# Performance work log

Measured on AMD Instinct MI355X. Metric: run time of the kernel, lower is better.

Reference implementation:

```python
import jax, jax.numpy as jnp
import numpy as np

EPS = 1e-6  # torch F.normalize eps


def setup_inputs() -> dict:
    key = jax.random.key(0)
    ks = jax.random.split(key, 9)
    B, C, H, W = 2, 256, 64, 64
    nH, dk, dv = 4, 64, 64
    s = 0.05  # weight scale for numerical stability
    return {
        "x": jax.random.normal(ks[0], (B, C, H, W), jnp.float32),
        "Wq": jax.random.normal(ks[1], (nH, dk, C), jnp.float32) * s,
        "bq": jax.random.normal(ks[2], (nH, dk), jnp.float32) * s,
        "Wk": jax.random.normal(ks[3], (nH, dk, C), jnp.float32) * s,
        "bk": jax.random.normal(ks[4], (nH, dk), jnp.float32) * s,
        "Wv": jax.random.normal(ks[5], (nH, dv, C), jnp.float32) * s,
        "bv": jax.random.normal(ks[6], (nH, dv), jnp.float32) * s,
        "Wm": jax.random.normal(ks[7], (C, nH * dv), jnp.float32) * s,
        "bm": jax.random.normal(ks[8], (C,), jnp.float32) * s,
    }


def _l2norm(t):
    # torch F.normalize along channel dim (axis=2 here: [B,H,dk,L])
    n = jnp.sqrt(jnp.sum(t * t, axis=2, keepdims=True))
    return t / jnp.maximum(n, EPS)


def reference(x, Wq, bq, Wk, bk, Wv, bv, Wm, bm):
    B, C, H, W = x.shape
    nH = Wq.shape[0]
    L = H * W
    xf = x.reshape(B, C, L)  # 1x1 conv == channel matmul on flattened spatial
    # per-head projections: [B, nH, d, L]
    Q = jnp.einsum('bcl,hdc->bhdl', xf, Wq) + bq[None, :, :, None]
    K = jnp.einsum('bcl,hdc->bhdl', xf, Wk) + bk[None, :, :, None]
    V = jnp.einsum('bcl,hvc->bhvl', xf, Wv) + bv[None, :, :, None]
    Q = _l2norm(Q)
    K = _l2norm(K)
    # cosine-similarity scores A[b,h,i,j] = sum_d Q[b,h,d,i] K[b,h,d,j]
    A = jnp.einsum('bhdi,bhdj->bhij', Q, K)
    A = jax.nn.softmax(A, axis=-1)
    # R[b,h,v,i] = sum_j A[b,h,i,j] V[b,h,v,j]
    R = jnp.einsum('bhij,bhvj->bhvi', A, V)
    # concat heads along channels -> [B, nH*dv, L]
    Rc = R.reshape(B, nH * V.shape[2], L)
    out = jnp.einsum('bcl,oc->bol', Rc, Wm) + bm[None, :, None]
    out = out.reshape(B, C, H, W) + x  # residual
    return out
```

## Files before the change

kernel.cpp:

```cpp
#include <hip/hip_runtime.h>
#include <hip/hip_bf16.h>
#include <cstdint>
#include <cstddef>

typedef __bf16 bf16;
typedef bf16 bf16x8 __attribute__((ext_vector_type(8)));
typedef bf16 bf16x4 __attribute__((ext_vector_type(4)));
typedef bf16 bf16x2 __attribute__((ext_vector_type(2)));
typedef float f32x4 __attribute__((ext_vector_type(4)));
typedef float f32x16 __attribute__((ext_vector_type(16)));

#define MFMA16(A, B, Cc) __builtin_amdgcn_mfma_f32_16x16x32_bf16((A), (B), (Cc), 0, 0, 0)
#define MFMA32(A, B, Cc) __builtin_amdgcn_mfma_f32_32x32x16_bf16((A), (B), (Cc), 0, 0, 0)
#define GLD16(g, l)                                                          \
  __builtin_amdgcn_global_load_lds(                                          \
      (const __attribute__((address_space(1))) void*)(g),                    \
      (__attribute__((address_space(3))) void*)(l), 16, 0, 0)

static constexpr int L   = 4096;
static constexpr int CH  = 256;
static constexpr int NH  = 4;

static constexpr size_t OFF_WALL = 0;
static constexpr size_t OFF_WMB  = 393216;
static constexpr size_t OFF_BALL = 524288;
static constexpr size_t OFF_XT   = 528384;
static constexpr size_t OFF_QT   = 4722688;
static constexpr size_t OFF_KT   = 8916992;
static constexpr size_t OFF_VD   = 13111296;
static constexpr size_t OFF_RP1  = 17305600;
static constexpr size_t OFF_RP2  = 21499904;
static constexpr size_t OFF_RP3  = 25694208;
static constexpr size_t OFF_DP4  = 29888512;
static constexpr size_t OFF_DP2  = 21499904;
static constexpr size_t NEED4    = 30412800;

__global__ __launch_bounds__(256) void k_prep(
    const float* __restrict__ Wq, const float* __restrict__ Wk,
    const float* __restrict__ Wv, const float* __restrict__ bq,
    const float* __restrict__ bk, const float* __restrict__ bv,
    const float* __restrict__ Wm, const float* __restrict__ x,
    bf16* __restrict__ Wall, float* __restrict__ ball,
    bf16* __restrict__ Wmb, bf16* __restrict__ xT) {
  __shared__ float t[32][33];
  const int bid = blockIdx.x;
  const int tid = threadIdx.x;
  if (bid < 1027) {
    int id = bid * 256 + tid;
    if (id < 65536)        Wall[id] = (bf16)Wq[id];
    else if (id < 131072)  Wall[id] = (bf16)Wk[id - 65536];
    else if (id < 196608)  Wall[id] = (bf16)Wv[id - 131072];
    else if (id < 262144)  Wmb[id - 196608] = (bf16)Wm[id - 196608];
    else if (id < 262912) {
      int k = id - 262144;
      ball[k] = (k < 256) ? bq[k] : (k < 512) ? bk[k - 256] : bv[k - 512];
    }
  } else {
    const int id = bid - 1027;
    const int b = id >> 10;
    const int c0 = ((id >> 7) & 7) * 32;
    const int l0 = (id & 127) * 32;
    const int tx = tid & 31, ty = tid >> 5;
    #pragma unroll
    for (int i = 0; i < 4; ++i) {
      int c = c0 + ty + 8 * i;
      t[ty + 8 * i][tx] = x[((size_t)b * CH + c) * L + l0 + tx];
    }
    __syncthreads();
    #pragma unroll
    for (int i = 0; i < 4; ++i) {
      int l = l0 + ty + 8 * i;
      xT[((size_t)b * L + l) * CH + c0 + tx] = (bf16)t[tx][ty + 8 * i];
    }
  }
}

__global__ __launch_bounds__(256) void k_proj(
    const bf16* __restrict__ Wall, const float* __restrict__ ball,
    const bf16* __restrict__ xT, bf16* __restrict__ Qt,
    bf16* __restrict__ Kt, bf16* __restrict__ Vd) {
  const int b = blockIdx.z, strip = blockIdx.y, lt = blockIdx.x;
  const int w = threadIdx.x >> 6;
  const int lane = threadIdx.x & 63;
  const int lo = lane & 15, g = lane >> 4;
  const int l0 = lt * 256 + w * 64;

  const bf16* wbase = Wall + (size_t)strip * 64 * CH;
  const bf16* xbase = xT + (size_t)b * L * CH;

  f32x4 acc[4][4];
  #pragma unroll
  for (int m = 0; m < 4; ++m)
    #pragma unroll
    for (int n = 0; n < 4; ++n) acc[m][n] = (f32x4){0.f, 0.f, 0.f, 0.f};

  #pragma unroll
  for (int kc = 0; kc < 8; ++kc) {
    bf16x8 aw[4], bx[4];
    #pragma unroll
    for (int m = 0; m < 4; ++m)
      aw[m] = *(const bf16x8*)(wbase + (size_t)(16 * m + lo) * CH + kc * 32 + g * 8);
    #pragma unroll
    for (int n = 0; n < 4; ++n)
      bx[n] = *(const bf16x8*)(xbase + (size_t)(l0 + 16 * n + lo) * CH + kc * 32 + g * 8);
    #pragma unroll
    for (int m = 0; m < 4; ++m)
      #pragma unroll
      for (int n = 0; n < 4; ++n) acc[m][n] = MFMA16(aw[m], bx[n], acc[m][n]);
  }

  #pragma unroll
  for (int m = 0; m < 4; ++m)
    #pragma unroll
    for (int r = 0; r < 4; ++r) {
      float bias = ball[strip * 64 + 16 * m + 4 * g + r];
      #pragma unroll
      for (int n = 0; n < 4; ++n) acc[m][n][r] += bias;
    }

  if (strip < 8) {
    #pragma unroll
    for (int n = 0; n < 4; ++n) {
      float ss = 0.f;
      #pragma unroll
      for (int m = 0; m < 4; ++m)
        #pragma unroll
        for (int r = 0; r < 4; ++r) ss += acc[m][n][r] * acc[m][n][r];
      ss += __shfl_xor(ss, 16);
      ss += __shfl_xor(ss, 32);
      float sc = 1.f / fmaxf(sqrtf(ss), 1e-6f);
      #pragma unroll
      for (int m = 0; m < 4; ++m)
        #pragma unroll
        for (int r = 0; r < 4; ++r) acc[m][n][r] *= sc;
    }
    bf16* dst = (strip < 4) ? Qt : Kt;
    const int h = strip & 3;
    #pragma unroll
    for (int n = 0; n < 4; ++n) {
      const int l = l0 + 16 * n + lo;
      #pragma unroll
      for (int m = 0; m < 4; ++m) {
        size_t base = ((size_t)(b * NH + h) * L + l) * 64 + 16 * m + 4 * g;
        bf16x2 v01, v23;
        v01[0] = (bf16)acc[m][n][0]; v01[1] = (bf16)acc[m][n][1];
        v23[0] = (bf16)acc[m][n][2]; v23[1] = (bf16)acc[m][n][3];
        *(bf16x2*)(dst + base)     = v01;
        *(bf16x2*)(dst + base + 2) = v23;
      }
    }
  } else {
    const int h = strip - 8;
    const int lop = (lo & 3) | ((lo & 4) << 1) | ((lo & 8) >> 1);
    #pragma unroll
    for (int m = 0; m < 4; ++m)
      #pragma unroll
      for (int r = 0; r < 4; ++r) {
        const int d = 16 * m + 4 * g + r;
        #pragma unroll
        for (int n = 0; n < 4; ++n) {
          const int l = l0 + 16 * n + lop;
          Vd[((size_t)(b * NH + h) * 64 + d) * L + l] = (bf16)acc[m][n][r];
        }
      }
  }
}


#define STAGE(bb, j0)                                                          \
  {                                                                            \
    const char* gk0 = kbase + (size_t)((j0) + sr) * 128 + scS;                 \
    const char* gk1 = kbase + (size_t)((j0) + 32 + sr) * 128 + scS;            \
    const char* gv0 = vbase + (size_t)sr * 8192 + (size_t)(j0) * 2 + scS;      \
    const char* gv1 = vbase + (size_t)(32 + sr) * 8192 + (size_t)(j0) * 2 + scS; \
    GLD16(gk0, kbuf[bb] + tid * 16);                                           \
    GLD16(gk1, kbuf[bb] + 4096 + tid * 16);                                    \
    GLD16(gv0, vbuf[bb] + tid * 16);                                           \
    GLD16(gv1, vbuf[bb] + 4096 + tid * 16);                                    \
  }

#define COMPUTE(bb)                                                            \
  {                                                                            \
    const char* kb = kbuf[bb];                                                 \
    const char* vb = vbuf[bb];                                                 \
    _Pragma("unroll") for (int jb = 0; jb < 2; ++jb) {                         \
      bf16x8 kf[4], vf[2][2];                                                  \
      _Pragma("unroll") for (int f = 0; f < 4; ++f)                            \
        kf[f] = *(const bf16x8*)(kb + (32 * jb + ln) * 128 +                   \
                                 ((32 * f + 16 * hi) ^ sw));                   \
      _Pragma("unroll") for (int dvb = 0; dvb < 2; ++dvb)                      \
        _Pragma("unroll") for (int c = 0; c < 2; ++c)                          \
          vf[dvb][c] = *(const bf16x8*)(vb + (32 * dvb + ln) * 128 +           \
                                        ((64 * jb + 32 * c + 16 * hi) ^ sw));  \
      _Pragma("unroll") for (int qb = 0; qb < 2; ++qb) {                       \
        f32x16 z;                                                              \
        _Pragma("unroll") for (int r = 0; r < 16; ++r) z[r] = 0.f;             \
        _Pragma("unroll") for (int f = 0; f < 4; ++f)                          \
          z = MFMA32(kf[f], qf[qb][f], z);                                     \
        float p[16];                                                           \
        _Pragma("unroll") for (int r = 0; r < 16; ++r) p[r] = __expf(z[r]);    \
        float t0 = (p[0] + p[1]) + (p[2] + p[3]);                              \
        float t1 = (p[4] + p[5]) + (p[6] + p[7]);                              \
        float t2 = (p[8] + p[9]) + (p[10] + p[11]);                            \
        float t3 = (p[12] + p[13]) + (p[14] + p[15]);                          \
        den[qb] += (t0 + t1) + (t2 + t3);                                      \
        bf16x8 pf0, pf1;                                                       \
        _Pragma("unroll") for (int e = 0; e < 8; ++e) {                        \
          pf0[e] = (bf16)p[e];                                                 \
          pf1[e] = (bf16)p[8 + e];                                             \
        }                                                                      \
        _Pragma("unroll") for (int dvb = 0; dvb < 2; ++dvb) {                  \
          racc[qb][dvb] = MFMA32(pf0, vf[dvb][0], racc[qb][dvb]);              \
          racc[qb][dvb] = MFMA32(pf1, vf[dvb][1], racc[qb][dvb]);              \
        }                                                                      \
      }                                                                        \
    }                                                                          \
  }

template <int JS>
__global__ __launch_bounds__(256, 2) void k_attn(
    const bf16* __restrict__ Qt, const bf16* __restrict__ Kt,
    const bf16* __restrict__ Vd, bf16* __restrict__ R0,
    bf16* __restrict__ R1, bf16* __restrict__ R2, bf16* __restrict__ R3,
    float* __restrict__ D0, float* __restrict__ D1,
    float* __restrict__ D2, float* __restrict__ D3) {
  const int id = blockIdx.x;
  const int bh = id & 7;
  const int qt = (id >> 3) & 15;
  const int js = id >> 7;
  const int tid = threadIdx.x;
  const int w = tid >> 6;
  const int lane = tid & 63;
  const int ln = lane & 31, hi = lane >> 5;
  const int sw = (ln & 7) << 4;
  const int i0 = qt * 256 + w * 64;

  __shared__ __align__(16) char kbuf[2][8192];
  __shared__ __align__(16) char vbuf[2][8192];

  const char* kbase = (const char*)(Kt + (size_t)bh * L * 64);
  const char* vbase = (const char*)(Vd + (size_t)bh * 64 * L);

  const int sr = tid >> 3;
  const int sc = (tid & 7) * 16;
  const int scS = sc ^ ((sr & 7) << 4);

  const bf16* qbp = Qt + ((size_t)bh * L + i0) * 64;
  bf16x8 qf[2][4];
  #pragma unroll
  for (int qb = 0; qb < 2; ++qb)
    #pragma unroll
    for (int f = 0; f < 4; ++f)
      qf[qb][f] = *(const bf16x8*)(qbp + (size_t)(32 * qb + ln) * 64 + 16 * f + 8 * hi);

  f32x16 racc[2][2];
  #pragma unroll
  for (int qb = 0; qb < 2; ++qb)
    #pragma unroll
    for (int dvb = 0; dvb < 2; ++dvb)
      #pragma unroll
      for (int r = 0; r < 16; ++r) racc[qb][dvb][r] = 0.f;
  float den[2] = {0.f, 0.f};

  const int jbeg = js * (L / JS);
  const int nt = (L / JS) / 64;

  STAGE(0, jbeg)
  __syncthreads();
  for (int it = 0; it < nt; ++it) {
    const int bb = it & 1;
    if (it + 1 < nt) STAGE(bb ^ 1, jbeg + (it + 1) * 64)
    COMPUTE(bb)
    __syncthreads();
  }

  #pragma unroll
  for (int qb = 0; qb < 2; ++qb) den[qb] += __shfl_xor(den[qb], 32);

  bf16* rp = (js == 0) ? R0 : (js == 1) ? R1 : (js == 2) ? R2 : R3;
  float* dp = (js == 0) ? D0 : (js == 1) ? D1 : (js == 2) ? D2 : D3;

  if (hi == 0) {
    #pragma unroll
    for (int qb = 0; qb < 2; ++qb)
      dp[(size_t)bh * L + i0 + 32 * qb + ln] = den[qb];
  }
  #pragma unroll
  for (int qb = 0; qb < 2; ++qb)
    #pragma unroll
    for (int dvb = 0; dvb < 2; ++dvb)
      #pragma unroll
      for (int r = 0; r < 16; ++r) {
        const int q = 32 * qb + (r & 3) + 8 * (r >> 2) + 4 * hi;
        rp[((size_t)bh * L + i0 + q) * 64 + 32 * dvb + ln] = (bf16)racc[qb][dvb][r];
      }
}

template <int JS>
__global__ __launch_bounds__(256) void k_out(
    const bf16* __restrict__ Wmb, const bf16* __restrict__ R0,
    const bf16* __restrict__ R1, const bf16* __restrict__ R2,
    const bf16* __restrict__ R3, const float* __restrict__ D0,
    const float* __restrict__ D1, const float* __restrict__ D2,
    const float* __restrict__ D3, const float* __restrict__ x,
    const float* __restrict__ bm, float* __restrict__ out) {
  const int b = blockIdx.y, lt = blockIdx.x;
  const int w = threadIdx.x >> 6;
  const int lane = threadIdx.x & 63;
  const int lo = lane & 15, g = lane >> 4;
  const int o0 = w * 64, l0 = lt * 32;

  float invd[2][4];
  #pragma unroll
  for (int n = 0; n < 2; ++n) {
    const int l = l0 + 16 * n + lo;
    #pragma unroll
    for (int h = 0; h < 4; ++h) {
      const size_t di = (size_t)(b * NH + h) * L + l;
      float dd = D0[di] + D1[di];
      if (JS == 4) dd += D2[di] + D3[di];
      invd[n][h] = 1.0f / dd;
    }
  }

  f32x4 acc[4][2];
  #pragma unroll
  for (int m = 0; m < 4; ++m)
    #pragma unroll
    for (int n = 0; n < 2; ++n) acc[m][n] = (f32x4){0.f, 0.f, 0.f, 0.f};

  #pragma unroll
  for (int kc = 0; kc < 8; ++kc) {
    bf16x8 aw[4], bx[2];
    #pragma unroll
    for (int m = 0; m < 4; ++m)
      aw[m] = *(const bf16x8*)(Wmb + (size_t)(o0 + 16 * m + lo) * CH + kc * 32 + g * 8);
    const int h = kc >> 1;
    #pragma unroll
    for (int n = 0; n < 2; ++n) {
      const size_t base = ((size_t)(b * NH + h) * L + (l0 + 16 * n + lo)) * 64 +
                          (kc & 1) * 32 + 8 * g;
      bf16x8 r0 = *(const bf16x8*)(R0 + base);
      bf16x8 r1 = *(const bf16x8*)(R1 + base);
      const float iv = invd[n][h];
      if (JS == 4) {
        bf16x8 r2 = *(const bf16x8*)(R2 + base);
        bf16x8 r3 = *(const bf16x8*)(R3 + base);
        #pragma unroll
        for (int e = 0; e < 8; ++e) {
          float s = ((float)r0[e] + (float)r1[e]) + ((float)r2[e] + (float)r3[e]);
          bx[n][e] = (bf16)(s * iv);
        }
      } else {
        #pragma unroll
        for (int e = 0; e < 8; ++e)
          bx[n][e] = (bf16)(((float)r0[e] + (float)r1[e]) * iv);
      }
    }
    #pragma unroll
    for (int m = 0; m < 4; ++m)
      #pragma unroll
      for (int n = 0; n < 2; ++n) acc[m][n] = MFMA16(aw[m], bx[n], acc[m][n]);
  }

  #pragma unroll
  for (int m = 0; m < 4; ++m)
    #pragma unroll
    for (int r = 0; r < 4; ++r) {
      const int o = o0 + 16 * m + 4 * g + r;
      const float bias = bm[o];
      #pragma unroll
      for (int n = 0; n < 2; ++n) {
        const int l = l0 + 16 * n + lo;
        size_t idx = ((size_t)b * CH + o) * (size_t)L + l;
        out[idx] = acc[m][n][r] + bias + x[idx];
      }
    }
}

extern "C" void kernel_launch(void* const* d_in, const int* in_sizes, int n_in,
                              void* d_out, int out_size, void* d_ws, size_t ws_size,
                              hipStream_t stream) {
  const float* x  = (const float*)d_in[0];
  const float* Wq = (const float*)d_in[1];
  const float* bq = (const float*)d_in[2];
  const float* Wk = (const float*)d_in[3];
  const float* bk = (const float*)d_in[4];
  const float* Wv = (const float*)d_in[5];
  const float* bv = (const float*)d_in[6];
  const float* Wm = (const float*)d_in[7];
  const float* bm = (const float*)d_in[8];
  float* out = (float*)d_out;

  char* ws = (char*)d_ws;
  bf16*  Wall = (bf16*)(ws + OFF_WALL);
  bf16*  Wmb  = (bf16*)(ws + OFF_WMB);
  float* ball = (float*)(ws + OFF_BALL);
  bf16*  xT   = (bf16*)(ws + OFF_XT);
  bf16*  Qt   = (bf16*)(ws + OFF_QT);
  bf16*  Kt   = (bf16*)(ws + OFF_KT);
  bf16*  Vd   = (bf16*)(ws + OFF_VD);

  bf16* Rp0 = (bf16*)(ws + OFF_XT);
  bf16* Rp1 = (bf16*)(ws + OFF_RP1);

  k_prep<<<3075, 256, 0, stream>>>(Wq, Wk, Wv, bq, bk, bv, Wm, x, Wall, ball, Wmb, xT);
  k_proj<<<dim3(16, 12, 2), 256, 0, stream>>>(Wall, ball, xT, Qt, Kt, Vd);

  if (ws_size >= NEED4) {
    bf16*  Rp2 = (bf16*)(ws + OFF_RP2);
    bf16*  Rp3 = (bf16*)(ws + OFF_RP3);
    float* Dp  = (float*)(ws + OFF_DP4);
    float* D0 = Dp, *D1 = Dp + 32768, *D2 = Dp + 65536, *D3 = Dp + 98304;
    k_attn<4><<<512, 256, 0, stream>>>(Qt, Kt, Vd, Rp0, Rp1, Rp2, Rp3, D0, D1, D2, D3);
    k_out<4><<<dim3(128, 2), 256, 0, stream>>>(Wmb, Rp0, Rp1, Rp2, Rp3, D0, D1, D2, D3,
                                               x, bm, out);
  } else {
    float* Dp = (float*)(ws + OFF_DP2);
    float* D0 = Dp, *D1 = Dp + 32768;
    k_attn<2><<<256, 256, 0, stream>>>(Qt, Kt, Vd, Rp0, Rp1, nullptr, nullptr,
                                       D0, D1, nullptr, nullptr);
    k_out<2><<<dim3(128, 2), 256, 0, stream>>>(Wmb, Rp0, Rp1, nullptr, nullptr,
                                               D0, D1, nullptr, nullptr, x, bm, out);
  }
}
```

Baseline: 90.94 us.

## Triple-buffer attention K/V staging and halve projection tile width

```diff
diff --git a/kernel.cpp b/kernel.cpp
--- a/kernel.cpp
+++ b/kernel.cpp
@@ -83,30 +83,30 @@
   const int w = threadIdx.x >> 6;
   const int lane = threadIdx.x & 63;
   const int lo = lane & 15, g = lane >> 4;
-  const int l0 = lt * 256 + w * 64;
+  const int l0 = lt * 128 + w * 32;
 
   const bf16* wbase = Wall + (size_t)strip * 64 * CH;
   const bf16* xbase = xT + (size_t)b * L * CH;
 
-  f32x4 acc[4][4];
+  f32x4 acc[4][2];
   #pragma unroll
   for (int m = 0; m < 4; ++m)
     #pragma unroll
-    for (int n = 0; n < 4; ++n) acc[m][n] = (f32x4){0.f, 0.f, 0.f, 0.f};
+    for (int n = 0; n < 2; ++n) acc[m][n] = (f32x4){0.f, 0.f, 0.f, 0.f};
 
   #pragma unroll
   for (int kc = 0; kc < 8; ++kc) {
-    bf16x8 aw[4], bx[4];
+    bf16x8 aw[4], bx[2];
     #pragma unroll
     for (int m = 0; m < 4; ++m)
       aw[m] = *(const bf16x8*)(wbase + (size_t)(16 * m + lo) * CH + kc * 32 + g * 8);
     #pragma unroll
-    for (int n = 0; n < 4; ++n)
+    for (int n = 0; n < 2; ++n)
       bx[n] = *(const bf16x8*)(xbase + (size_t)(l0 + 16 * n + lo) * CH + kc * 32 + g * 8);
     #pragma unroll
     for (int m = 0; m < 4; ++m)
       #pragma unroll
-      for (int n = 0; n < 4; ++n) acc[m][n] = MFMA16(aw[m], bx[n], acc[m][n]);
+      for (int n = 0; n < 2; ++n) acc[m][n] = MFMA16(aw[m], bx[n], acc[m][n]);
   }
 
   #pragma unroll
@@ -115,12 +115,12 @@
     for (int r = 0; r < 4; ++r) {
       float bias = ball[strip * 64 + 16 * m + 4 * g + r];
       #pragma unroll
-      for (int n = 0; n < 4; ++n) acc[m][n][r] += bias;
+      for (int n = 0; n < 2; ++n) acc[m][n][r] += bias;
     }
 
   if (strip < 8) {
     #pragma unroll
-    for (int n = 0; n < 4; ++n) {
+    for (int n = 0; n < 2; ++n) {
       float ss = 0.f;
       #pragma unroll
       for (int m = 0; m < 4; ++m)
@@ -137,7 +137,7 @@
     bf16* dst = (strip < 4) ? Qt : Kt;
     const int h = strip & 3;
     #pragma unroll
-    for (int n = 0; n < 4; ++n) {
+    for (int n = 0; n < 2; ++n) {
       const int l = l0 + 16 * n + lo;
       #pragma unroll
       for (int m = 0; m < 4; ++m) {
@@ -158,7 +158,7 @@
       for (int r = 0; r < 4; ++r) {
         const int d = 16 * m + 4 * g + r;
         #pragma unroll
-        for (int n = 0; n < 4; ++n) {
+        for (int n = 0; n < 2; ++n) {
           const int l = l0 + 16 * n + lop;
           Vd[((size_t)(b * NH + h) * 64 + d) * L + l] = (bf16)acc[m][n][r];
         }
@@ -167,22 +167,22 @@
 }
 
 
-#define STAGE(bb, j0)                                                          \
+#define STAGE(kdst, vdst, j0)                                                  \
   {                                                                            \
     const char* gk0 = kbase + (size_t)((j0) + sr) * 128 + scS;                 \
     const char* gk1 = kbase + (size_t)((j0) + 32 + sr) * 128 + scS;            \
     const char* gv0 = vbase + (size_t)sr * 8192 + (size_t)(j0) * 2 + scS;      \
     const char* gv1 = vbase + (size_t)(32 + sr) * 8192 + (size_t)(j0) * 2 + scS; \
-    GLD16(gk0, kbuf[bb] + tid * 16);                                           \
-    GLD16(gk1, kbuf[bb] + 4096 + tid * 16);                                    \
-    GLD16(gv0, vbuf[bb] + tid * 16);                                           \
-    GLD16(gv1, vbuf[bb] + 4096 + tid * 16);                                    \
-  }
-
-#define COMPUTE(bb)                                                            \
+    GLD16(gk0, (kdst) + tid * 16);                                             \
+    GLD16(gk1, (kdst) + 4096 + tid * 16);                                      \
+    GLD16(gv0, (vdst) + tid * 16);                                             \
+    GLD16(gv1, (vdst) + 4096 + tid * 16);                                      \
+  }
+
+#define COMPUTE(kb_, vb_)                                                      \
   {                                                                            \
-    const char* kb = kbuf[bb];                                                 \
-    const char* vb = vbuf[bb];                                                 \
+    const char* kb = (kb_);                                                    \
+    const char* vb = (vb_);                                                    \
     _Pragma("unroll") for (int jb = 0; jb < 2; ++jb) {                         \
       bf16x8 kf[4], vf[2][2];                                                  \
       _Pragma("unroll") for (int f = 0; f < 4; ++f)                            \
@@ -235,8 +235,8 @@
   const int sw = (ln & 7) << 4;
   const int i0 = qt * 256 + w * 64;
 
-  __shared__ __align__(16) char kbuf[2][8192];
-  __shared__ __align__(16) char vbuf[2][8192];
+  __shared__ __align__(16) char kbuf[3][8192];
+  __shared__ __align__(16) char vbuf[3][8192];
 
   const char* kbase = (const char*)(Kt + (size_t)bh * L * 64);
   const char* vbase = (const char*)(Vd + (size_t)bh * 64 * L);
@@ -265,13 +265,24 @@
   const int jbeg = js * (L / JS);
   const int nt = (L / JS) / 64;
 
-  STAGE(0, jbeg)
-  __syncthreads();
+  STAGE(kbuf[0], vbuf[0], jbeg)
+  STAGE(kbuf[1], vbuf[1], jbeg + 64)
+  asm volatile("s_waitcnt vmcnt(4)" ::: "memory");
+  __builtin_amdgcn_s_barrier();
+
+  int bc = 0, bs = 2;
   for (int it = 0; it < nt; ++it) {
-    const int bb = it & 1;
-    if (it + 1 < nt) STAGE(bb ^ 1, jbeg + (it + 1) * 64)
-    COMPUTE(bb)
-    __syncthreads();
+    if (it + 2 < nt) STAGE(kbuf[bs], vbuf[bs], jbeg + (it + 2) * 64)
+    COMPUTE(kbuf[bc], vbuf[bc])
+    if (it + 1 < nt) {
+      if (it + 2 < nt)
+        asm volatile("s_waitcnt vmcnt(4)" ::: "memory");
+      else
+        asm volatile("s_waitcnt vmcnt(0)" ::: "memory");
+      __builtin_amdgcn_s_barrier();
+    }
+    bc = (bc == 2) ? 0 : bc + 1;
+    bs = (bs == 2) ? 0 : bs + 1;
   }
 
   #pragma unroll
@@ -405,7 +416,7 @@
   bf16* Rp1 = (bf16*)(ws + OFF_RP1);
 
   k_prep<<<3075, 256, 0, stream>>>(Wq, Wk, Wv, bq, bk, bv, Wm, x, Wall, ball, Wmb, xT);
-  k_proj<<<dim3(16, 12, 2), 256, 0, stream>>>(Wall, ball, xT, Qt, Kt, Vd);
+  k_proj<<<dim3(32, 12, 2), 256, 0, stream>>>(Wall, ball, xT, Qt, Kt, Vd);
 
   if (ws_size >= NEED4) {
     bf16*  Rp2 = (bf16*)(ws + OFF_RP2);
```

After: 91.41 us. Within noise of the previous version (+0.5%).
